# Performance work log

Measured on AMD Instinct MI355X. Metric: run time of the kernel, lower is better.

The kernel has to match this reference:

```python
import jax, jax.numpy as jnp
import numpy as np
from jax import lax

NPG = 61      # nodes (electrodes) per graph, hard-coded by 61*hidden reshape
B = 128       # graphs per batch
L = 160       # raw signal length -> final conv length 1
NF = 64       # num_features
HC = 128      # hidden_channels
NCLS = 4


def setup_inputs() -> dict:
    key = jax.random.key(0)
    ks = jax.random.split(key, 16)
    N = B * NPG
    # fully-connected (no self-loops) edges within each graph -> 3660 edges/graph
    a = np.repeat(np.arange(NPG), NPG)
    b = np.tile(np.arange(NPG), NPG)
    m = a != b
    sl, dl = a[m], b[m]
    off = (np.arange(B) * NPG)[:, None]
    edge_index = np.stack([(sl[None] + off).ravel(), (dl[None] + off).ravel()]).astype(np.int64)
    batch = np.repeat(np.arange(B), NPG).astype(np.int64)

    def rn(k, shape, fan_in):
        return jax.random.normal(k, shape, jnp.float32) / np.sqrt(fan_in).astype(np.float32)

    return dict(
        x=jax.random.normal(ks[0], (N, L), jnp.float32),
        edge_index=jnp.asarray(edge_index),
        batch=jnp.asarray(batch),
        edge_features=jax.random.normal(ks[1], (edge_index.shape[1], 3), jnp.float32),
        conv_w0=rn(ks[2], (NF, 1, 7), 7.0), conv_b0=jnp.zeros((NF,), jnp.float32),
        conv_w1=rn(ks[3], (NF, NF, 5), NF * 5.0), conv_b1=jnp.zeros((NF,), jnp.float32),
        conv_w2=rn(ks[4], (NF, NF, 3), NF * 3.0), conv_b2=jnp.zeros((NF,), jnp.float32),
        bn1_g=jnp.ones((NF,), jnp.float32), bn1_b=jnp.zeros((NF,), jnp.float32),
        g_w0=rn(ks[5], (NF, HC), float(NF)), g_b0=jnp.zeros((HC,), jnp.float32),
        g_w1=rn(ks[6], (HC, HC), float(HC)), g_b1=jnp.zeros((HC,), jnp.float32),
        g_w2=rn(ks[7], (HC, HC), float(HC)), g_b2=jnp.zeros((HC,), jnp.float32),
        bn2_g=jnp.ones((HC,), jnp.float32), bn2_b=jnp.zeros((HC,), jnp.float32),
        lin_w0=rn(ks[8], (NPG * HC, HC), float(NPG * HC)), lin_b0=jnp.zeros((HC,), jnp.float32),
        lin_w1=rn(ks[9], (HC, HC), float(HC)), lin_b1=jnp.zeros((HC,), jnp.float32),
        lin_w2=rn(ks[10], (HC, NCLS), float(HC)), lin_b2=jnp.zeros((NCLS,), jnp.float32),
        edge_w=rn(ks[11], (3, 1), 3.0), edge_b=jnp.zeros((1,), jnp.float32),
    )


def _conv1d(x, w, b, pad):
    # x: [N, Cin, L], w: [Cout, Cin, K]
    y = lax.conv_general_dilated(x, w, (1,), [(pad, pad)], dimension_numbers=('NCH', 'OIH', 'NCH'))
    return y + b[None, :, None]


def _maxpool7(x):
    n = x.shape[-1] // 7
    return x[..., : n * 7].reshape(x.shape[0], x.shape[1], n, 7).max(-1)


def _bn(x, g, b):
    # BatchNorm1d in training mode: biased batch statistics
    m = x.mean(0)
    v = x.var(0)
    return (x - m) * lax.rsqrt(v + 1e-5) * g + b


def _forward(x, edge_features, conv_w0, conv_b0, conv_w1, conv_b1, conv_w2, conv_b2,
             bn1_g, bn1_b, g_w0, g_b0, g_w1, g_b1, g_w2, g_b2, bn2_g, bn2_b,
             lin_w0, lin_b0, lin_w1, lin_b1, lin_w2, lin_b2, edge_w, edge_b,
             edge_index, batch):
    N = x.shape[0]
    nb = N // NPG  # == batch.max()+1 for contiguous graph layout
    # tanh-gated edge weights
    ew = jnp.tanh(edge_features @ edge_w + edge_b)            # [E, 1]
    # Conv1d feature extractor: [N,1,160] -> [N,NF,1]
    h = x[:, None, :]
    h = _maxpool7(jax.nn.relu(_conv1d(h, conv_w0, conv_b0, 0)))   # [N,NF,22]
    h = jax.nn.relu(_conv1d(h, conv_w1, conv_b1, 2))               # [N,NF,22]
    h = _maxpool7(h)                                               # [N,NF,3]
    h = _conv1d(h, conv_w2, conv_b2, 0)[:, :, 0]                   # [N,NF]
    h = _bn(h, bn1_g, bn1_b)
    # Edge-weighted GCN hops (MyzConv): lin -> gather src -> scale -> scatter-add dst
    src, dst = edge_index[0], edge_index[1]
    for w, bs, act in ((g_w0, g_b0, True), (g_w1, g_b1, True), (g_w2, g_b2, False)):
        hw = h @ w + bs                                            # [N,HC]
        msg = ew * hw[src]                                         # [E,HC]
        h = jax.ops.segment_sum(msg, dst, num_segments=N)
        if act:
            h = jax.nn.relu(h)
    h = _bn(h, bn2_g, bn2_b)
    # MLP classifier over concatenated node features per graph
    h = h.reshape(nb, NPG * HC)
    h = jax.nn.relu(h @ lin_w0 + lin_b0)
    h = jax.nn.relu(h @ lin_w1 + lin_b1)
    h = h @ lin_w2 + lin_b2
    return jax.nn.log_softmax(h, -1), ew.reshape(nb, -1).T


def reference(x, edge_index, batch, edge_features, conv_w0, conv_b0, conv_w1, conv_b1,
              conv_w2, conv_b2, bn1_g, bn1_b, g_w0, g_b0, g_w1, g_b1, g_w2, g_b2,
              bn2_g, bn2_b, lin_w0, lin_b0, lin_w1, lin_b1, lin_w2, lin_b2, edge_w, edge_b):
    return _forward(x, edge_features, conv_w0, conv_b0, conv_w1, conv_b1, conv_w2, conv_b2,
                    bn1_g, bn1_b, g_w0, g_b0, g_w1, g_b1, g_w2, g_b2, bn2_g, bn2_b,
                    lin_w0, lin_b0, lin_w1, lin_b1, lin_w2, lin_b2, edge_w, edge_b,
                    edge_index, batch)
```

## Files before the change

### kernel.cpp

```cpp
#include <hip/hip_runtime.h>
#include <math.h>

#define NPGN 61
#define NGRAPH 128
#define NNODES (NPGN*NGRAPH)
#define EPG 3660

typedef float float4v __attribute__((ext_vector_type(4)));
typedef short bf16x8 __attribute__((ext_vector_type(8)));
typedef unsigned short u16;

__device__ __forceinline__ u16 f2bf(float v){
  union { float f; unsigned u; } x; x.f = v;
  unsigned r = (x.u + 0x7FFFu + ((x.u >> 16) & 1u)) >> 16;
  return (u16)r;
}
__device__ __forceinline__ float bf2f(unsigned u){
  union { unsigned u; float f; } x; x.u = u << 16;
  return x.f;
}

__global__ __launch_bounds__(256) void k_prep(const float* __restrict__ w0,
    const float* __restrict__ w1, const float* __restrict__ w2,
    const float* __restrict__ gw0, const float* __restrict__ gw1, const float* __restrict__ gw2,
    const float* __restrict__ lw0,
    float* __restrict__ w0t, u16* __restrict__ w1b, u16* __restrict__ w2b,
    u16* __restrict__ gwt0, u16* __restrict__ gwt1, u16* __restrict__ gwt2,
    u16* __restrict__ lw0t){
  __shared__ __align__(16) u16 tile[32*132];
  int b = blockIdx.x, tid = threadIdx.x;
  if (b < 290){
    int idx = b*256 + tid;
    if (idx < 20480){
      int f = idx / 320, r = idx - f*320;
      int kk = r >> 6, c = r & 63;
      w1b[idx] = f2bf(w1[f*320 + c*5 + kk]);
    } else if (idx < 32768){
      int j = idx - 20480; w2b[j] = f2bf(w2[j]);
    } else if (idx < 40960){
      int j = idx - 32768; int jj = j >> 6, k = j & 63; gwt0[j] = f2bf(gw0[k*128 + jj]);
    } else if (idx < 57344){
      int j = idx - 40960; int jj = j >> 7, k = j & 127; gwt1[j] = f2bf(gw1[k*128 + jj]);
    } else if (idx < 73728){
      int j = idx - 57344; int jj = j >> 7, k = j & 127; gwt2[j] = f2bf(gw2[k*128 + jj]);
    } else if (idx < 74176){
      int j = idx - 73728; int k = j >> 6, f = j & 63; w0t[j] = w0[f*7 + k];
    }
  } else {
    int bb = b - 290;
    int i = bb >> 2, oq = bb & 3;
    for (int idx = tid; idx < 4096; idx += 256){
      int k = idx >> 5, ol = idx & 31;
      tile[ol*132 + k] = f2bf(lw0[((size_t)i*128 + k)*128 + oq*32 + ol]);
    }
    __syncthreads();
    unsigned* dst = (unsigned*)lw0t;
    for (int idx = tid; idx < 2048; idx += 256){
      int ol = idx >> 6, kw = idx & 63;
      unsigned v = (unsigned)tile[ol*132 + 2*kw] | ((unsigned)tile[ol*132 + 2*kw + 1] << 16);
      dst[((size_t)i*128 + oq*32 + ol)*64 + kw] = v;
    }
  }
}

#define A0T_STR 72
#define C1_STR 40
__global__ __launch_bounds__(256) void k_conv(const float* __restrict__ x,
    const float* __restrict__ w0t, const float* __restrict__ b0,
    const u16* __restrict__ w1b, const float* __restrict__ b1,
    const u16* __restrict__ w2b, const float* __restrict__ b2,
    float* __restrict__ h0, float* __restrict__ stat1p){
  int w = threadIdx.x >> 6, lane = threadIdx.x & 63;
  int tid = threadIdx.x;
  int n = blockIdx.x*4 + w;
  __shared__ __align__(16) u16 a0t_s[4][36*A0T_STR];
  __shared__ __align__(16) u16 a1k_s[4][208];
  __shared__ float hstat[4][128];
  u16* a0t = a0t_s[w];
  u16* a1k = a1k_s[w];

  const float* xrow = x + (size_t)__builtin_amdgcn_readfirstlane(n)*160;

  float w0r[7];
  #pragma unroll
  for (int k = 0; k < 7; k++) w0r[k] = w0t[k*64 + lane];
  float b0f = b0[lane];
  #pragma unroll
  for (int rp = 0; rp < 36; rp++)
    if (rp < 2 || rp >= 24) a0t[rp*A0T_STR + lane] = 0;

  #pragma unroll 2
  for (int qp = 0; qp < 11; qp++){
    float win[20];
    #pragma unroll
    for (int j = 0; j < 20; j++) win[j] = xrow[14*qp + j];
    float m0, m1;
    #pragma unroll
    for (int r = 0; r < 7; r++){
      float s = w0r[0]*win[r];
      #pragma unroll
      for (int k = 1; k < 7; k++) s += w0r[k]*win[r+k];
      m0 = r ? fmaxf(m0, s) : s;
    }
    #pragma unroll
    for (int r = 7; r < 14; r++){
      float s = w0r[0]*win[r];
      #pragma unroll
      for (int k = 1; k < 7; k++) s += w0r[k]*win[r+k];
      m1 = (r > 7) ? fmaxf(m1, s) : s;
    }
    a0t[(2 + 2*qp)*A0T_STR + lane] = f2bf(fmaxf(m0 + b0f, 0.f));
    a0t[(3 + 2*qp)*A0T_STR + lane] = f2bf(fmaxf(m1 + b0f, 0.f));
  }

  int q = lane >> 4, r16 = lane & 15;
  float4v acc[4][2];
  #pragma unroll
  for (int mt = 0; mt < 4; mt++)
    #pragma unroll
    for (int nt = 0; nt < 2; nt++)
      acc[mt][nt] = (float4v){0.f,0.f,0.f,0.f};
  #pragma unroll 1
  for (int ks = 0; ks < 10; ks++){
    int kk = ks >> 1;
    int cbase = (ks & 1)*32 + q*8;
    bf16x8 af[4];
    #pragma unroll
    for (int mt = 0; mt < 4; mt++)
      af[mt] = *(const bf16x8*)(w1b + (16*mt + r16)*320 + ks*32 + q*8);
    bf16x8 bv[2];
    #pragma unroll
    for (int nt = 0; nt < 2; nt++)
      bv[nt] = *(const bf16x8*)(a0t + (r16 + 16*nt + kk)*A0T_STR + cbase);
    #pragma unroll
    for (int mt = 0; mt < 4; mt++)
      #pragma unroll
      for (int nt = 0; nt < 2; nt++)
        acc[mt][nt] = __builtin_amdgcn_mfma_f32_16x16x32_bf16(af[mt], bv[nt], acc[mt][nt], 0, 0, 0);
  }

  u16* c1 = a0t;
  #pragma unroll
  for (int mt = 0; mt < 4; mt++){
    float4 bb = *(const float4*)(b1 + 16*mt + 4*q);
    #pragma unroll
    for (int reg = 0; reg < 4; reg++){
      int m = 16*mt + q*4 + reg;
      float bv_ = ((const float*)&bb)[reg];
      c1[m*C1_STR + r16] = f2bf(fmaxf(acc[mt][0][reg] + bv_, 0.f));
      if (r16 <= 4)
        c1[m*C1_STR + 16 + r16] = f2bf(fmaxf(acc[mt][1][reg] + bv_, 0.f));
    }
  }

  {
    bf16x8 f0 = *(const bf16x8*)(c1 + lane*C1_STR);
    bf16x8 f1 = *(const bf16x8*)(c1 + lane*C1_STR + 8);
    bf16x8 f2 = *(const bf16x8*)(c1 + lane*C1_STR + 16);
    float v[24];
    #pragma unroll
    for (int j = 0; j < 8; j++){
      v[j]    = bf2f((u16)f0[j]);
      v[8+j]  = bf2f((u16)f1[j]);
      v[16+j] = bf2f((u16)f2[j]);
    }
    #pragma unroll
    for (int t = 0; t < 3; t++){
      float m = v[t*7];
      #pragma unroll
      for (int r = 1; r < 7; r++) m = fmaxf(m, v[t*7+r]);
      a1k[lane*3 + t] = f2bf(m);
    }
  }

  float4v acc2[4];
  #pragma unroll
  for (int mt = 0; mt < 4; mt++) acc2[mt] = (float4v){0.f,0.f,0.f,0.f};
  #pragma unroll
  for (int ks = 0; ks < 6; ks++){
    bf16x8 bs = *(const bf16x8*)(a1k + ks*32 + q*8);
    #pragma unroll
    for (int mt = 0; mt < 4; mt++){
      bf16x8 af = *(const bf16x8*)(w2b + (16*mt + r16)*192 + ks*32 + q*8);
      acc2[mt] = __builtin_amdgcn_mfma_f32_16x16x32_bf16(af, bs, acc2[mt], 0, 0, 0);
    }
  }
  if (r16 == 0){
    #pragma unroll
    for (int mt = 0; mt < 4; mt++)
      #pragma unroll
      for (int reg = 0; reg < 4; reg++){
        int f = 16*mt + 4*q + reg;
        float v = acc2[mt][reg] + b2[f];
        h0[(size_t)n*64 + f] = v;
        hstat[w][f] = v;
        hstat[w][64 + f] = v*v;
      }
  }
  __syncthreads();
  if (tid < 128){
    float a = hstat[0][tid] + hstat[1][tid] + hstat[2][tid] + hstat[3][tid];
    atomicAdd(&stat1p[(blockIdx.x & 31)*128 + tid], a);
  }
}

#define EW_STR 72
#define HS_STR 136
#define HWT_STR 72
__global__ __launch_bounds__(512) void k_gnn(const float* __restrict__ h0,
    const float* __restrict__ stat1p,
    const float* __restrict__ bn1g, const float* __restrict__ bn1b,
    const u16* __restrict__ gwt0, const float* __restrict__ gb0,
    const u16* __restrict__ gwt1, const float* __restrict__ gb1,
    const u16* __restrict__ gwt2, const float* __restrict__ gb2,
    const float* __restrict__ ef, const float* __restrict__ eww,
    const float* __restrict__ ewb, float* __restrict__ out2,
    u16* __restrict__ hB, float* __restrict__ stat2p){
  int g = blockIdx.x, tid = threadIdx.x;
  int w = tid >> 6, lane = tid & 63, q = lane >> 4, r16 = lane & 15;
  int dt = w & 3, jh = w >> 2;
  __shared__ u16 hs[64*HS_STR];
  __shared__ u16 hwT[128*HWT_STR];
  __shared__ u16 ewl[64*EW_STR];
  __shared__ float bsc[64], bsh[64];
  __shared__ float st2[256];

  bf16x8 af0[2], af1[4], af2[4];
  #pragma unroll
  for (int ks = 0; ks < 2; ks++)
    af0[ks] = *(const bf16x8*)(gwt0 + (16*w + r16)*64 + ks*32 + q*8);
  #pragma unroll
  for (int ks = 0; ks < 4; ks++)
    af1[ks] = *(const bf16x8*)(gwt1 + (16*w + r16)*128 + ks*32 + q*8);
  #pragma unroll
  for (int ks = 0; ks < 4; ks++)
    af2[ks] = *(const bf16x8*)(gwt2 + (16*w + r16)*128 + ks*32 + q*8);
  float4 b40 = *(const float4*)(gb0 + 16*w + 4*q);
  float4 b41 = *(const float4*)(gb1 + 16*w + 4*q);
  float4 b42 = *(const float4*)(gb2 + 16*w + 4*q);

  if (tid < 64){
    float s = 0.f, s2 = 0.f;
    #pragma unroll
    for (int r = 0; r < 32; r++){
      s  += stat1p[r*128 + tid];
      s2 += stat1p[r*128 + 64 + tid];
    }
    float m = s*(1.f/NNODES), v = s2*(1.f/NNODES) - m*m;
    float sc = rsqrtf(v + 1e-5f)*bn1g[tid];
    bsc[tid] = sc; bsh[tid] = bn1b[tid] - m*sc;
  }
  if (tid < 256) st2[tid] = 0.f;
  {
    unsigned* td = (unsigned*)ewl;
    for (int idx = tid; idx < 64*EW_STR/2; idx += 512) td[idx] = 0;
  }
  {
    unsigned* hsd = (unsigned*)hs;
    for (int idx = tid; idx < 3*(HS_STR/2); idx += 512){
      int rr = 61 + idx/(HS_STR/2), cc = idx%(HS_STR/2);
      hsd[rr*(HS_STR/2) + cc] = 0;
    }
  }
  __syncthreads();

  {
    float v0 = eww[0], v1 = eww[1], v2 = eww[2], bb = ewb[0];
    const float* efg = ef + (size_t)g*EPG*3;
    for (int idx = tid; idx < EPG; idx += 512){
      const float* p = efg + idx*3;
      float v = tanhf(p[0]*v0 + p[1]*v1 + p[2]*v2 + bb);
      int s = idx/60, r = idx - s*60;
      int d = r + (r >= s ? 1 : 0);
      ewl[d*EW_STR + s] = f2bf(v);
      out2[(size_t)idx*128 + g] = v;
    }
  }
  {
    unsigned* hsd = (unsigned*)hs;
    for (int idx = tid; idx < 61*32; idx += 512){
      int i = idx >> 5, kw = idx & 31;
      float2 hv = *(const float2*)(h0 + ((size_t)g*61 + i)*64 + kw*2);
      int k0 = kw*2;
      float a = hv.x*bsc[k0] + bsh[k0];
      float b = hv.y*bsc[k0+1] + bsh[k0+1];
      hsd[i*(HS_STR/2) + kw] = (unsigned)f2bf(a) | ((unsigned)f2bf(b) << 16);
    }
  }
  __syncthreads();
  bf16x8 ewf[2];
  #pragma unroll
  for (int ks = 0; ks < 2; ks++)
    ewf[ks] = *(const bf16x8*)(ewl + (16*dt + r16)*EW_STR + ks*32 + q*8);

  #pragma unroll
  for (int nt = 0; nt < 4; nt++){
    float4v acc = {b40.x, b40.y, b40.z, b40.w};
    #pragma unroll
    for (int ks = 0; ks < 2; ks++){
      bf16x8 bv = *(const bf16x8*)(hs + (nt*16 + r16)*HS_STR + ks*32 + q*8);
      acc = __builtin_amdgcn_mfma_f32_16x16x32_bf16(af0[ks], bv, acc, 0, 0, 0);
    }
    #pragma unroll
    for (int r = 0; r < 4; r++)
      hwT[(16*w + 4*q + r)*HWT_STR + nt*16 + r16] = f2bf(acc[r]);
  }
  __syncthreads();
  #pragma unroll
  for (int nt = 0; nt < 4; nt++){
    int j = (jh*4 + nt)*16;
    float4v acc = {0.f,0.f,0.f,0.f};
    #pragma unroll
    for (int ks = 0; ks < 2; ks++){
      bf16x8 bv = *(const bf16x8*)(hwT + (j + r16)*HWT_STR + ks*32 + q*8);
      acc = __builtin_amdgcn_mfma_f32_16x16x32_bf16(ewf[ks], bv, acc, 0, 0, 0);
    }
    #pragma unroll
    for (int r = 0; r < 4; r++){
      int d = 16*dt + 4*q + r;
      hs[d*HS_STR + j + r16] = f2bf(fmaxf(acc[r], 0.f));
    }
  }
  __syncthreads();

  #pragma unroll
  for (int nt = 0; nt < 4; nt++){
    float4v acc = {b41.x, b41.y, b41.z, b41.w};
    #pragma unroll
    for (int ks = 0; ks < 4; ks++){
      bf16x8 bv = *(const bf16x8*)(hs + (nt*16 + r16)*HS_STR + ks*32 + q*8);
      acc = __builtin_amdgcn_mfma_f32_16x16x32_bf16(af1[ks], bv, acc, 0, 0, 0);
    }
    #pragma unroll
    for (int r = 0; r < 4; r++)
      hwT[(16*w + 4*q + r)*HWT_STR + nt*16 + r16] = f2bf(acc[r]);
  }
  __syncthreads();
  #pragma unroll
  for (int nt = 0; nt < 4; nt++){
    int j = (jh*4 + nt)*16;
    float4v acc = {0.f,0.f,0.f,0.f};
    #pragma unroll
    for (int ks = 0; ks < 2; ks++){
      bf16x8 bv = *(const bf16x8*)(hwT + (j + r16)*HWT_STR + ks*32 + q*8);
      acc = __builtin_amdgcn_mfma_f32_16x16x32_bf16(ewf[ks], bv, acc, 0, 0, 0);
    }
    #pragma unroll
    for (int r = 0; r < 4; r++){
      int d = 16*dt + 4*q + r;
      hs[d*HS_STR + j + r16] = f2bf(fmaxf(acc[r], 0.f));
    }
  }
  __syncthreads();

  #pragma unroll
  for (int nt = 0; nt < 4; nt++){
    float4v acc = {b42.x, b42.y, b42.z, b42.w};
    #pragma unroll
    for (int ks = 0; ks < 4; ks++){
      bf16x8 bv = *(const bf16x8*)(hs + (nt*16 + r16)*HS_STR + ks*32 + q*8);
      acc = __builtin_amdgcn_mfma_f32_16x16x32_bf16(af2[ks], bv, acc, 0, 0, 0);
    }
    #pragma unroll
    for (int r = 0; r < 4; r++)
      hwT[(16*w + 4*q + r)*HWT_STR + nt*16 + r16] = f2bf(acc[r]);
  }
  __syncthreads();
  #pragma unroll
  for (int nt = 0; nt < 4; nt++){
    int j = (jh*4 + nt)*16;
    float4v acc = {0.f,0.f,0.f,0.f};
    #pragma unroll
    for (int ks = 0; ks < 2; ks++){
      bf16x8 bv = *(const bf16x8*)(hwT + (j + r16)*HWT_STR + ks*32 + q*8);
      acc = __builtin_amdgcn_mfma_f32_16x16x32_bf16(ewf[ks], bv, acc, 0, 0, 0);
    }
    float cs = 0.f, cq = 0.f;
    #pragma unroll
    for (int r = 0; r < 4; r++){
      int d = 16*dt + 4*q + r;
      if (d < 61){
        float v = acc[r];
        hB[((size_t)g*61 + d)*128 + j + r16] = f2bf(v);
        cs += v; cq += v*v;
      }
    }
    int col = j + r16;
    atomicAdd(&st2[col], cs);
    atomicAdd(&st2[128 + col], cq);
  }
  __syncthreads();
  if (tid < 256) stat2p[(size_t)tid*128 + g] = st2[tid];
}

#define AS_STR 136
__global__ __launch_bounds__(256) void k_mlp0(const u16* __restrict__ hB,
    const float* __restrict__ stat2p,
    const float* __restrict__ bn2g, const float* __restrict__ bn2b,
    const u16* __restrict__ lw0t, float* __restrict__ y0pre){
  int bi = blockIdx.x; int i = bi >> 2, sub = bi & 3;
  int oh = sub & 1, gh = sub >> 1;
  int tid = threadIdx.x, w = tid >> 6, lane = tid & 63, q = lane >> 4, r16 = lane & 15;
  __shared__ u16 As[64*AS_STR];
  __shared__ float sc2[128], sh2[128];
  if (tid < 128){
    float4v sa = {0,0,0,0}, sb = {0,0,0,0};
    #pragma unroll
    for (int r = 0; r < 32; r++){
      sa += *(const float4v*)(stat2p + (size_t)tid*128 + r*4);
      sb += *(const float4v*)(stat2p + (size_t)(128 + tid)*128 + r*4);
    }
    float s = sa[0]+sa[1]+sa[2]+sa[3], s2 = sb[0]+sb[1]+sb[2]+sb[3];
    float m = s*(1.f/NNODES), v = s2*(1.f/NNODES) - m*m;
    float sc = rsqrtf(v + 1e-5f)*bn2g[tid];
    sc2[tid] = sc; sh2[tid] = bn2b[tid] - m*sc;
  }
  __syncthreads();
  {
    const unsigned* hbd = (const unsigned*)hB;
    unsigned* asd = (unsigned*)As;
    for (int idx = tid; idx < 4096; idx += 256){
      int gg = gh*64 + (idx >> 6), kw = idx & 63;
      unsigned pv = hbd[((size_t)gg*61 + i)*64 + kw];
      int k0 = kw*2;
      float a = bf2f(pv & 0xffffu)*sc2[k0] + sh2[k0];
      float b = bf2f(pv >> 16)*sc2[k0+1] + sh2[k0+1];
      asd[(idx >> 6)*(AS_STR/2) + kw] = (unsigned)f2bf(a) | ((unsigned)f2bf(b) << 16);
    }
  }
  __syncthreads();
  const u16* wbase = lw0t + ((size_t)i*128 + oh*64)*128;
  bf16x8 af[4];
  #pragma unroll
  for (int ks = 0; ks < 4; ks++)
    af[ks] = *(const bf16x8*)(As + (16*w + r16)*AS_STR + ks*32 + q*8);
  #pragma unroll
  for (int nt = 0; nt < 4; nt++){
    float4v acc = {0.f,0.f,0.f,0.f};
    #pragma unroll
    for (int ks = 0; ks < 4; ks++){
      bf16x8 bv = *(const bf16x8*)(wbase + (size_t)(nt*16 + r16)*128 + ks*32 + q*8);
      acc = __builtin_amdgcn_mfma_f32_16x16x32_bf16(af[ks], bv, acc, 0, 0, 0);
    }
    #pragma unroll
    for (int r = 0; r < 4; r++){
      int g = gh*64 + 16*w + 4*q + r;
      atomicAdd(&y0pre[(size_t)g*128 + oh*64 + nt*16 + r16], acc[r]);
    }
  }
}

__global__ __launch_bounds__(128) void k_mlp1(const float* __restrict__ y0pre,
    const float* __restrict__ lb0, const float* __restrict__ W1,
    const float* __restrict__ lb1, const float* __restrict__ W2,
    const float* __restrict__ lb2, float* __restrict__ out){
  int g = blockIdx.x, o = threadIdx.x;
  __shared__ float y0[128], y1[128], red[128];
  y0[o] = fmaxf(y0pre[(size_t)g*128 + o] + lb0[o], 0.f);
  __syncthreads();
  float a = lb1[o];
  #pragma unroll 8
  for (int k = 0; k < 128; k++) a += y0[k]*W1[k*128 + o];
  y1[o] = fmaxf(a, 0.f);
  __syncthreads();
  int c = o & 3, kb = o >> 2;
  float a2 = 0.f;
  #pragma unroll
  for (int j = 0; j < 4; j++){
    int k = kb + 32*j;
    a2 += y1[k]*W2[k*4 + c];
  }
  red[o] = a2;
  __syncthreads();
  #pragma unroll
  for (int off = 64; off >= 4; off >>= 1){
    if (o < off) red[o] += red[o + off];
    __syncthreads();
  }
  if (o == 0){
    float v0 = red[0]+lb2[0], v1 = red[1]+lb2[1], v2 = red[2]+lb2[2], v3 = red[3]+lb2[3];
    float m = fmaxf(fmaxf(v0,v1), fmaxf(v2,v3));
    float lse = m + logf(expf(v0-m)+expf(v1-m)+expf(v2-m)+expf(v3-m));
    out[g*4+0]=v0-lse; out[g*4+1]=v1-lse; out[g*4+2]=v2-lse; out[g*4+3]=v3-lse;
  }
}

extern "C" void kernel_launch(void* const* d_in, const int* in_sizes, int n_in,
                              void* d_out, int out_size, void* d_ws, size_t ws_size,
                              hipStream_t stream){
  const float* x    = (const float*)d_in[0];
  const float* ef   = (const float*)d_in[3];
  const float* cw0  = (const float*)d_in[4];
  const float* cb0  = (const float*)d_in[5];
  const float* cw1  = (const float*)d_in[6];
  const float* cb1  = (const float*)d_in[7];
  const float* cw2  = (const float*)d_in[8];
  const float* cb2  = (const float*)d_in[9];
  const float* bn1g = (const float*)d_in[10];
  const float* bn1b = (const float*)d_in[11];
  const float* gw0  = (const float*)d_in[12];
  const float* gb0  = (const float*)d_in[13];
  const float* gw1  = (const float*)d_in[14];
  const float* gb1  = (const float*)d_in[15];
  const float* gw2  = (const float*)d_in[16];
  const float* gb2  = (const float*)d_in[17];
  const float* bn2g = (const float*)d_in[18];
  const float* bn2b = (const float*)d_in[19];
  const float* lw0  = (const float*)d_in[20];
  const float* lb0  = (const float*)d_in[21];
  const float* lw1  = (const float*)d_in[22];
  const float* lb1  = (const float*)d_in[23];
  const float* lw2  = (const float*)d_in[24];
  const float* lb2  = (const float*)d_in[25];
  const float* eww  = (const float*)d_in[26];
  const float* ewb  = (const float*)d_in[27];
  float* out = (float*)d_out;

  float* ws   = (float*)d_ws;
  float* w1s  = ws;
  float* w2s  = w1s + 10240;
  float* w0t  = w2s + 6144;
  float* gws0 = w0t + 448;
  float* gws1 = gws0 + 4096;
  float* gws2 = gws1 + 8192;
  float* h0   = gws2 + 8192;
  float* hBs  = h0 + 499712;
  float* lw0s = hBs + 499712;
  float* accs = lw0s + 499712;

  u16* w1b    = (u16*)w1s;
  u16* w2b    = (u16*)w2s;
  u16* gwt0   = (u16*)gws0;
  u16* gwt1   = (u16*)gws1;
  u16* gwt2   = (u16*)gws2;
  u16* hB     = (u16*)hBs;
  u16* lw0t   = (u16*)lw0s;
  float* stat1p = accs;
  float* y0pre  = accs + 4096;
  float* stat2p = accs + 20480;

  hipMemsetAsync(accs, 0, 20480*sizeof(float), stream);
  k_prep <<<534, 256, 0, stream>>>(cw0, cw1, cw2, gw0, gw1, gw2, lw0,
                                   w0t, w1b, w2b, gwt0, gwt1, gwt2, lw0t);
  k_conv <<<NNODES/4, 256, 0, stream>>>(x, w0t, cb0, w1b, cb1, w2b, cb2, h0, stat1p);
  k_gnn  <<<NGRAPH, 512, 0, stream>>>(h0, stat1p, bn1g, bn1b,
                                      gwt0, gb0, gwt1, gb1, gwt2, gb2,
                                      ef, eww, ewb, out + 512, hB, stat2p);
  k_mlp0 <<<NPGN*4, 256, 0, stream>>>(hB, stat2p, bn2g, bn2b, lw0t, y0pre);
  k_mlp1 <<<NGRAPH, 128, 0, stream>>>(y0pre, lb0, lw1, lb1, lw2, lb2, out);
}
```

Before: 225.3 us.

## Split each conv node across two waves instead of one wave per node

```diff
diff --git a/kernel.cpp b/kernel.cpp
--- a/kernel.cpp
+++ b/kernel.cpp
@@ -65,32 +65,32 @@
 
 #define A0T_STR 72
 #define C1_STR 40
-__global__ __launch_bounds__(256) void k_conv(const float* __restrict__ x,
+__global__ __launch_bounds__(128, 8) void k_conv(const float* __restrict__ x,
     const float* __restrict__ w0t, const float* __restrict__ b0,
     const u16* __restrict__ w1b, const float* __restrict__ b1,
     const u16* __restrict__ w2b, const float* __restrict__ b2,
     float* __restrict__ h0, float* __restrict__ stat1p){
   int w = threadIdx.x >> 6, lane = threadIdx.x & 63;
-  int tid = threadIdx.x;
-  int n = blockIdx.x*4 + w;
-  __shared__ __align__(16) u16 a0t_s[4][36*A0T_STR];
-  __shared__ __align__(16) u16 a1k_s[4][208];
-  __shared__ float hstat[4][128];
-  u16* a0t = a0t_s[w];
-  u16* a1k = a1k_s[w];
-
-  const float* xrow = x + (size_t)__builtin_amdgcn_readfirstlane(n)*160;
+  int n = blockIdx.x;
+  __shared__ __align__(16) u16 a0t[36*A0T_STR];
+  __shared__ __align__(16) u16 a1k[208];
+
+  const float* xrow = x + (size_t)n*160;
 
   float w0r[7];
   #pragma unroll
   for (int k = 0; k < 7; k++) w0r[k] = w0t[k*64 + lane];
   float b0f = b0[lane];
-  #pragma unroll
-  for (int rp = 0; rp < 36; rp++)
-    if (rp < 2 || rp >= 24) a0t[rp*A0T_STR + lane] = 0;
+
+  #pragma unroll
+  for (int i = 0; i < 7; i++){
+    int ii = w*7 + i;
+    int rp = (ii < 2) ? ii : ii + 22;
+    a0t[rp*A0T_STR + lane] = 0;
+  }
 
   #pragma unroll 2
-  for (int qp = 0; qp < 11; qp++){
+  for (int qp = w; qp < 11; qp += 2){
     float win[20];
     #pragma unroll
     for (int j = 0; j < 20; j++) win[j] = xrow[14*qp + j];
@@ -112,95 +112,104 @@
     a0t[(2 + 2*qp)*A0T_STR + lane] = f2bf(fmaxf(m0 + b0f, 0.f));
     a0t[(3 + 2*qp)*A0T_STR + lane] = f2bf(fmaxf(m1 + b0f, 0.f));
   }
+  __syncthreads();
 
   int q = lane >> 4, r16 = lane & 15;
-  float4v acc[4][2];
-  #pragma unroll
-  for (int mt = 0; mt < 4; mt++)
+  float4v acc[2][2];
+  #pragma unroll
+  for (int t = 0; t < 2; t++)
     #pragma unroll
     for (int nt = 0; nt < 2; nt++)
-      acc[mt][nt] = (float4v){0.f,0.f,0.f,0.f};
+      acc[t][nt] = (float4v){0.f,0.f,0.f,0.f};
   #pragma unroll 1
   for (int ks = 0; ks < 10; ks++){
     int kk = ks >> 1;
     int cbase = (ks & 1)*32 + q*8;
-    bf16x8 af[4];
-    #pragma unroll
-    for (int mt = 0; mt < 4; mt++)
-      af[mt] = *(const bf16x8*)(w1b + (16*mt + r16)*320 + ks*32 + q*8);
+    bf16x8 af[2];
+    #pragma unroll
+    for (int t = 0; t < 2; t++)
+      af[t] = *(const bf16x8*)(w1b + (16*(2*w + t) + r16)*320 + ks*32 + q*8);
     bf16x8 bv[2];
     #pragma unroll
     for (int nt = 0; nt < 2; nt++)
       bv[nt] = *(const bf16x8*)(a0t + (r16 + 16*nt + kk)*A0T_STR + cbase);
     #pragma unroll
-    for (int mt = 0; mt < 4; mt++)
+    for (int t = 0; t < 2; t++)
       #pragma unroll
       for (int nt = 0; nt < 2; nt++)
-        acc[mt][nt] = __builtin_amdgcn_mfma_f32_16x16x32_bf16(af[mt], bv[nt], acc[mt][nt], 0, 0, 0);
-  }
+        acc[t][nt] = __builtin_amdgcn_mfma_f32_16x16x32_bf16(af[t], bv[nt], acc[t][nt], 0, 0, 0);
+  }
+  __syncthreads();
 
   u16* c1 = a0t;
   #pragma unroll
-  for (int mt = 0; mt < 4; mt++){
+  for (int t = 0; t < 2; t++){
+    int mt = 2*w + t;
     float4 bb = *(const float4*)(b1 + 16*mt + 4*q);
     #pragma unroll
     for (int reg = 0; reg < 4; reg++){
       int m = 16*mt + q*4 + reg;
       float bv_ = ((const float*)&bb)[reg];
-      c1[m*C1_STR + r16] = f2bf(fmaxf(acc[mt][0][reg] + bv_, 0.f));
+      c1[m*C1_STR + r16] = f2bf(fmaxf(acc[t][0][reg] + bv_, 0.f));
       if (r16 <= 4)
-        c1[m*C1_STR + 16 + r16] = f2bf(fmaxf(acc[mt][1][reg] + bv_, 0.f));
-    }
-  }
-
-  {
+        c1[m*C1_STR + 16 + r16] = f2bf(fmaxf(acc[t][1][reg] + bv_, 0.f));
+    }
+  }
+  __syncthreads();
+
+  if (w == 0){
     bf16x8 f0 = *(const bf16x8*)(c1 + lane*C1_STR);
     bf16x8 f1 = *(const bf16x8*)(c1 + lane*C1_STR + 8);
-    bf16x8 f2 = *(const bf16x8*)(c1 + lane*C1_STR + 16);
-    float v[24];
-    #pragma unroll
-    for (int j = 0; j < 8; j++){
-      v[j]    = bf2f((u16)f0[j]);
-      v[8+j]  = bf2f((u16)f1[j]);
-      v[16+j] = bf2f((u16)f2[j]);
-    }
-    #pragma unroll
-    for (int t = 0; t < 3; t++){
+    float v[14];
+    #pragma unroll
+    for (int j = 0; j < 8; j++) v[j] = bf2f((u16)f0[j]);
+    #pragma unroll
+    for (int j = 0; j < 6; j++) v[8+j] = bf2f((u16)f1[j]);
+    #pragma unroll
+    for (int t = 0; t < 2; t++){
       float m = v[t*7];
       #pragma unroll
       for (int r = 1; r < 7; r++) m = fmaxf(m, v[t*7+r]);
       a1k[lane*3 + t] = f2bf(m);
     }
-  }
-
-  float4v acc2[4];
-  #pragma unroll
-  for (int mt = 0; mt < 4; mt++) acc2[mt] = (float4v){0.f,0.f,0.f,0.f};
+  } else {
+    bf16x8 f1 = *(const bf16x8*)(c1 + lane*C1_STR + 8);
+    bf16x8 f2 = *(const bf16x8*)(c1 + lane*C1_STR + 16);
+    float v[7];
+    v[0] = bf2f((u16)f1[6]); v[1] = bf2f((u16)f1[7]);
+    #pragma unroll
+    for (int j = 0; j < 5; j++) v[2+j] = bf2f((u16)f2[j]);
+    float m = v[0];
+    #pragma unroll
+    for (int r = 1; r < 7; r++) m = fmaxf(m, v[r]);
+    a1k[lane*3 + 2] = f2bf(m);
+  }
+  __syncthreads();
+
+  float4v acc2[2];
+  #pragma unroll
+  for (int t = 0; t < 2; t++) acc2[t] = (float4v){0.f,0.f,0.f,0.f};
   #pragma unroll
   for (int ks = 0; ks < 6; ks++){
     bf16x8 bs = *(const bf16x8*)(a1k + ks*32 + q*8);
     #pragma unroll
-    for (int mt = 0; mt < 4; mt++){
-      bf16x8 af = *(const bf16x8*)(w2b + (16*mt + r16)*192 + ks*32 + q*8);
-      acc2[mt] = __builtin_amdgcn_mfma_f32_16x16x32_bf16(af, bs, acc2[mt], 0, 0, 0);
+    for (int t = 0; t < 2; t++){
+      bf16x8 af = *(const bf16x8*)(w2b + (16*(2*w + t) + r16)*192 + ks*32 + q*8);
+      acc2[t] = __builtin_amdgcn_mfma_f32_16x16x32_bf16(af, bs, acc2[t], 0, 0, 0);
     }
   }
   if (r16 == 0){
-    #pragma unroll
-    for (int mt = 0; mt < 4; mt++)
+    int bkt = n & 31;
+    #pragma unroll
+    for (int t = 0; t < 2; t++)
       #pragma unroll
       for (int reg = 0; reg < 4; reg++){
-        int f = 16*mt + 4*q + reg;
-        float v = acc2[mt][reg] + b2[f];
+        int f = 16*(2*w + t) + 4*q + reg;
+        float v = acc2[t][reg] + b2[f];
         h0[(size_t)n*64 + f] = v;
-        hstat[w][f] = v;
-        hstat[w][64 + f] = v*v;
+        atomicAdd(&stat1p[bkt*128 + f], v);
+        atomicAdd(&stat1p[bkt*128 + 64 + f], v*v);
       }
-  }
-  __syncthreads();
-  if (tid < 128){
-    float a = hstat[0][tid] + hstat[1][tid] + hstat[2][tid] + hstat[3][tid];
-    atomicAdd(&stat1p[(blockIdx.x & 31)*128 + tid], a);
   }
 }
 
@@ -542,7 +551,7 @@
   hipMemsetAsync(accs, 0, 20480*sizeof(float), stream);
   k_prep <<<534, 256, 0, stream>>>(cw0, cw1, cw2, gw0, gw1, gw2, lw0,
                                    w0t, w1b, w2b, gwt0, gwt1, gwt2, lw0t);
-  k_conv <<<NNODES/4, 256, 0, stream>>>(x, w0t, cb0, w1b, cb1, w2b, cb2, h0, stat1p);
+  k_conv <<<NNODES, 128, 0, stream>>>(x, w0t, cb0, w1b, cb1, w2b, cb2, h0, stat1p);
   k_gnn  <<<NGRAPH, 512, 0, stream>>>(h0, stat1p, bn1g, bn1b,
                                       gwt0, gb0, gwt1, gb1, gwt2, gb2,
                                       ef, eww, ewb, out + 512, hB, stat2p);
```

Measured after the change: 240.8 us. 6.9% more time.

## Split conv work across waves by output channels with register-resident weights

Applied to the files above, without the earlier changes.

```diff
diff --git a/kernel.cpp b/kernel.cpp
--- a/kernel.cpp
+++ b/kernel.cpp
@@ -64,143 +64,138 @@
 }
 
 #define A0T_STR 72
-#define C1_STR 40
+#define A0T_ROWS 36
+#define C1_STR 24
+#define NB 4
 __global__ __launch_bounds__(256) void k_conv(const float* __restrict__ x,
     const float* __restrict__ w0t, const float* __restrict__ b0,
     const u16* __restrict__ w1b, const float* __restrict__ b1,
     const u16* __restrict__ w2b, const float* __restrict__ b2,
     float* __restrict__ h0, float* __restrict__ stat1p){
   int w = threadIdx.x >> 6, lane = threadIdx.x & 63;
-  int tid = threadIdx.x;
-  int n = blockIdx.x*4 + w;
-  __shared__ __align__(16) u16 a0t_s[4][36*A0T_STR];
-  __shared__ __align__(16) u16 a1k_s[4][208];
-  __shared__ float hstat[4][128];
-  u16* a0t = a0t_s[w];
-  u16* a1k = a1k_s[w];
-
-  const float* xrow = x + (size_t)__builtin_amdgcn_readfirstlane(n)*160;
+  int q = lane >> 4, r16 = lane & 15;
+  __shared__ __align__(16) u16 a0t[A0T_ROWS*A0T_STR];
+  __shared__ __align__(16) u16 a1k[208];
+
+  bf16x8 wf1[10], wf2[6];
+  #pragma unroll
+  for (int ks = 0; ks < 10; ks++)
+    wf1[ks] = *(const bf16x8*)(w1b + (16*w + r16)*320 + ks*32 + q*8);
+  #pragma unroll
+  for (int ks = 0; ks < 6; ks++)
+    wf2[ks] = *(const bf16x8*)(w2b + (16*w + r16)*192 + ks*32 + q*8);
+  float4 b1v = *(const float4*)(b1 + 16*w + 4*q);
+  float4 b2v = *(const float4*)(b2 + 16*w + 4*q);
 
   float w0r[7];
   #pragma unroll
   for (int k = 0; k < 7; k++) w0r[k] = w0t[k*64 + lane];
   float b0f = b0[lane];
-  #pragma unroll
-  for (int rp = 0; rp < 36; rp++)
-    if (rp < 2 || rp >= 24) a0t[rp*A0T_STR + lane] = 0;
-
-  #pragma unroll 2
-  for (int qp = 0; qp < 11; qp++){
-    float win[20];
-    #pragma unroll
-    for (int j = 0; j < 20; j++) win[j] = xrow[14*qp + j];
-    float m0, m1;
-    #pragma unroll
-    for (int r = 0; r < 7; r++){
-      float s = w0r[0]*win[r];
+
+  a0t[(24 + w)*A0T_STR + lane] = 0;
+
+  float4v sacc = {0.f,0.f,0.f,0.f}, qacc = {0.f,0.f,0.f,0.f};
+
+  for (int i = 0; i < NB; i++){
+    int n = blockIdx.x*NB + i;
+    const float* xrow = x + (size_t)n*160;
+
+    if (w < 2) a0t[w*A0T_STR + lane] = 0;
+
+    for (int qp = w; qp < 11; qp += 4){
+      float win[20];
       #pragma unroll
-      for (int k = 1; k < 7; k++) s += w0r[k]*win[r+k];
-      m0 = r ? fmaxf(m0, s) : s;
-    }
-    #pragma unroll
-    for (int r = 7; r < 14; r++){
-      float s = w0r[0]*win[r];
+      for (int j = 0; j < 20; j++) win[j] = xrow[14*qp + j];
+      float m0, m1;
       #pragma unroll
-      for (int k = 1; k < 7; k++) s += w0r[k]*win[r+k];
-      m1 = (r > 7) ? fmaxf(m1, s) : s;
-    }
-    a0t[(2 + 2*qp)*A0T_STR + lane] = f2bf(fmaxf(m0 + b0f, 0.f));
-    a0t[(3 + 2*qp)*A0T_STR + lane] = f2bf(fmaxf(m1 + b0f, 0.f));
-  }
-
-  int q = lane >> 4, r16 = lane & 15;
-  float4v acc[4][2];
-  #pragma unroll
-  for (int mt = 0; mt < 4; mt++)
-    #pragma unroll
-    for (int nt = 0; nt < 2; nt++)
-      acc[mt][nt] = (float4v){0.f,0.f,0.f,0.f};
-  #pragma unroll 1
-  for (int ks = 0; ks < 10; ks++){
-    int kk = ks >> 1;
-    int cbase = (ks & 1)*32 + q*8;
-    bf16x8 af[4];
-    #pragma unroll
-    for (int mt = 0; mt < 4; mt++)
-      af[mt] = *(const bf16x8*)(w1b + (16*mt + r16)*320 + ks*32 + q*8);
-    bf16x8 bv[2];
-    #pragma unroll
-    for (int nt = 0; nt < 2; nt++)
-      bv[nt] = *(const bf16x8*)(a0t + (r16 + 16*nt + kk)*A0T_STR + cbase);
-    #pragma unroll
-    for (int mt = 0; mt < 4; mt++)
+      for (int r = 0; r < 7; r++){
+        float s = w0r[0]*win[r];
+        #pragma unroll
+        for (int k = 1; k < 7; k++) s += w0r[k]*win[r+k];
+        m0 = r ? fmaxf(m0, s) : s;
+      }
       #pragma unroll
-      for (int nt = 0; nt < 2; nt++)
-        acc[mt][nt] = __builtin_amdgcn_mfma_f32_16x16x32_bf16(af[mt], bv[nt], acc[mt][nt], 0, 0, 0);
-  }
-
-  u16* c1 = a0t;
-  #pragma unroll
-  for (int mt = 0; mt < 4; mt++){
-    float4 bb = *(const float4*)(b1 + 16*mt + 4*q);
+      for (int r = 7; r < 14; r++){
+        float s = w0r[0]*win[r];
+        #pragma unroll
+        for (int k = 1; k < 7; k++) s += w0r[k]*win[r+k];
+        m1 = (r > 7) ? fmaxf(m1, s) : s;
+      }
+      a0t[(2 + 2*qp)*A0T_STR + lane] = f2bf(fmaxf(m0 + b0f, 0.f));
+      a0t[(3 + 2*qp)*A0T_STR + lane] = f2bf(fmaxf(m1 + b0f, 0.f));
+    }
+    __syncthreads();
+
+    float4v acc0 = {0.f,0.f,0.f,0.f}, acc1 = {0.f,0.f,0.f,0.f};
+    #pragma unroll
+    for (int ks = 0; ks < 10; ks++){
+      int kk = ks >> 1;
+      int cbase = (ks & 1)*32 + q*8;
+      bf16x8 bv0 = *(const bf16x8*)(a0t + (r16 + kk)*A0T_STR + cbase);
+      bf16x8 bv1 = *(const bf16x8*)(a0t + (r16 + 16 + kk)*A0T_STR + cbase);
+      acc0 = __builtin_amdgcn_mfma_f32_16x16x32_bf16(wf1[ks], bv0, acc0, 0, 0, 0);
+      acc1 = __builtin_amdgcn_mfma_f32_16x16x32_bf16(wf1[ks], bv1, acc1, 0, 0, 0);
+    }
+    __syncthreads();
+
+    u16* c1 = a0t;
     #pragma unroll
     for (int reg = 0; reg < 4; reg++){
-      int m = 16*mt + q*4 + reg;
-      float bv_ = ((const float*)&bb)[reg];
-      c1[m*C1_STR + r16] = f2bf(fmaxf(acc[mt][0][reg] + bv_, 0.f));
+      int m = 16*w + q*4 + reg;
+      float bv_ = ((const float*)&b1v)[reg];
+      c1[m*C1_STR + r16] = f2bf(fmaxf(acc0[reg] + bv_, 0.f));
       if (r16 <= 4)
-        c1[m*C1_STR + 16 + r16] = f2bf(fmaxf(acc[mt][1][reg] + bv_, 0.f));
-    }
-  }
-
-  {
-    bf16x8 f0 = *(const bf16x8*)(c1 + lane*C1_STR);
-    bf16x8 f1 = *(const bf16x8*)(c1 + lane*C1_STR + 8);
-    bf16x8 f2 = *(const bf16x8*)(c1 + lane*C1_STR + 16);
-    float v[24];
-    #pragma unroll
-    for (int j = 0; j < 8; j++){
-      v[j]    = bf2f((u16)f0[j]);
-      v[8+j]  = bf2f((u16)f1[j]);
-      v[16+j] = bf2f((u16)f2[j]);
-    }
-    #pragma unroll
-    for (int t = 0; t < 3; t++){
-      float m = v[t*7];
+        c1[m*C1_STR + 16 + r16] = f2bf(fmaxf(acc1[reg] + bv_, 0.f));
+    }
+    __syncthreads();
+
+    if (w == (i & 3)){
+      bf16x8 f0 = *(const bf16x8*)(c1 + lane*C1_STR);
+      bf16x8 f1 = *(const bf16x8*)(c1 + lane*C1_STR + 8);
+      bf16x8 f2 = *(const bf16x8*)(c1 + lane*C1_STR + 16);
+      float v[24];
       #pragma unroll
-      for (int r = 1; r < 7; r++) m = fmaxf(m, v[t*7+r]);
-      a1k[lane*3 + t] = f2bf(m);
-    }
-  }
-
-  float4v acc2[4];
-  #pragma unroll
-  for (int mt = 0; mt < 4; mt++) acc2[mt] = (float4v){0.f,0.f,0.f,0.f};
-  #pragma unroll
-  for (int ks = 0; ks < 6; ks++){
-    bf16x8 bs = *(const bf16x8*)(a1k + ks*32 + q*8);
-    #pragma unroll
-    for (int mt = 0; mt < 4; mt++){
-      bf16x8 af = *(const bf16x8*)(w2b + (16*mt + r16)*192 + ks*32 + q*8);
-      acc2[mt] = __builtin_amdgcn_mfma_f32_16x16x32_bf16(af, bs, acc2[mt], 0, 0, 0);
-    }
-  }
-  if (r16 == 0){
-    #pragma unroll
-    for (int mt = 0; mt < 4; mt++)
+      for (int j = 0; j < 8; j++){
+        v[j]    = bf2f((u16)f0[j]);
+        v[8+j]  = bf2f((u16)f1[j]);
+        v[16+j] = bf2f((u16)f2[j]);
+      }
+      #pragma unroll
+      for (int t = 0; t < 3; t++){
+        float m = v[t*7];
+        #pragma unroll
+        for (int r = 1; r < 7; r++) m = fmaxf(m, v[t*7+r]);
+        a1k[lane*3 + t] = f2bf(m);
+      }
+    }
+    __syncthreads();
+
+    float4v acc2 = {0.f,0.f,0.f,0.f};
+    #pragma unroll
+    for (int ks = 0; ks < 6; ks++){
+      bf16x8 bs = *(const bf16x8*)(a1k + ks*32 + q*8);
+      acc2 = __builtin_amdgcn_mfma_f32_16x16x32_bf16(wf2[ks], bs, acc2, 0, 0, 0);
+    }
+    if (r16 == 0){
       #pragma unroll
       for (int reg = 0; reg < 4; reg++){
-        int f = 16*mt + 4*q + reg;
-        float v = acc2[mt][reg] + b2[f];
+        int f = 16*w + 4*q + reg;
+        float v = acc2[reg] + ((const float*)&b2v)[reg];
         h0[(size_t)n*64 + f] = v;
-        hstat[w][f] = v;
-        hstat[w][64 + f] = v*v;
+        sacc[reg] += v;
+        qacc[reg] += v*v;
       }
-  }
-  __syncthreads();
-  if (tid < 128){
-    float a = hstat[0][tid] + hstat[1][tid] + hstat[2][tid] + hstat[3][tid];
-    atomicAdd(&stat1p[(blockIdx.x & 31)*128 + tid], a);
+    }
+  }
+
+  if (r16 == 0){
+    int bkt = blockIdx.x & 31;
+    #pragma unroll
+    for (int reg = 0; reg < 4; reg++){
+      int f = 16*w + 4*q + reg;
+      atomicAdd(&stat1p[bkt*128 + f], sacc[reg]);
+      atomicAdd(&stat1p[bkt*128 + 64 + f], qacc[reg]);
+    }
   }
 }
 
@@ -542,7 +537,7 @@
   hipMemsetAsync(accs, 0, 20480*sizeof(float), stream);
   k_prep <<<534, 256, 0, stream>>>(cw0, cw1, cw2, gw0, gw1, gw2, lw0,
                                    w0t, w1b, w2b, gwt0, gwt1, gwt2, lw0t);
-  k_conv <<<NNODES/4, 256, 0, stream>>>(x, w0t, cb0, w1b, cb1, w2b, cb2, h0, stat1p);
+  k_conv <<<NNODES/NB, 256, 0, stream>>>(x, w0t, cb0, w1b, cb1, w2b, cb2, h0, stat1p);
   k_gnn  <<<NGRAPH, 512, 0, stream>>>(h0, stat1p, bn1g, bn1b,
                                       gwt0, gb0, gwt1, gb1, gwt2, gb2,
                                       ef, eww, ewb, out + 512, hB, stat2p);
```

Result: faster. 210.9 us (-6.4%).
